# Kernel tuning notes

Measured on AMD Instinct MI355X. Metric: run time of the kernel, lower is better.

## Reference

```python
import jax, jax.numpy as jnp
import numpy as np

B, N, NODE_DIM = 8, 128, 64
L, RES_DIM = 512, 1024
CG, CP = 128, 128
NUM_GNN_STEPS = 3
HID = CG + CP // 2  # interaction hidden = 192


def setup_inputs() -> dict:
    key = jax.random.key(0)
    ks = jax.random.split(key, 20)
    a = (jax.random.uniform(ks[0], (B, N, N)) < 0.05).astype(jnp.float32)
    adj = jnp.clip(a + jnp.swapaxes(a, 1, 2), 0.0, 1.0)
    adj = adj * (1.0 - jnp.eye(N, dtype=jnp.float32))
    nodes = jax.random.normal(ks[1], (B, N, NODE_DIM), dtype=jnp.float32)
    prot = jax.random.normal(ks[2], (B, L, RES_DIM), dtype=jnp.float32)
    s = 0.02
    inp = {
        "adj_mats": adj, "nodes": nodes, "protein_sequences": prot,
        "Wn": jax.random.normal(ks[3], (NODE_DIM, CG)) * s, "bn": jnp.zeros((CG,)),
        "Wg": jax.random.normal(ks[4], (CG, CG)) * s, "bg": jnp.zeros((CG,)),
        "Wr": jax.random.normal(ks[5], (RES_DIM, CP)) * s, "br": jnp.zeros((CP,)),
        "Wa": jax.random.normal(ks[6], (CG + CP, 1)) * s, "ba": jnp.zeros((1,)),
        "W1": jax.random.normal(ks[7], (CG + CP, HID)) * s, "b1": jnp.zeros((HID,)),
        "W2": jax.random.normal(ks[8], (HID, CG)) * s, "b2": jnp.zeros((CG,)),
        "Wo": jax.random.normal(ks[9], (CG, 1)) * s, "bo": jnp.zeros((1,)),
    }
    return inp


def reference(adj_mats, nodes, protein_sequences,
              Wn, bn, Wg, bg, Wr, br, Wa, ba, W1, b1, W2, b2, Wo, bo):
    # node compression: [B,N,CG]
    h = nodes @ Wn + bn
    deg = jnp.clip(jnp.sum(adj_mats, axis=-1), 1.0, None)        # [B,N]
    norm = deg ** -0.5                                           # [B,N]
    for i in range(NUM_GNN_STEPS):
        m = jnp.einsum('bij,bjc->bic', adj_mats, h * norm[..., None])
        h = (m * norm[..., None]) @ Wg + bg
        h = jnp.tanh(h) if i == NUM_GNN_STEPS - 1 else jax.nn.relu(h)
    # residue compression: [B,L,CP]
    r = protein_sequences @ Wr + br
    # MergeSnE1: all-pairs broadcast concat -> [B, N*L, CG+CP]
    cat = jnp.concatenate([
        jnp.broadcast_to(h[:, :, None, :], (B, N, L, CG)),
        jnp.broadcast_to(r[:, None, :, :], (B, N, L, CP)),
    ], axis=-1).reshape(B, N * L, CG + CP)
    # attention: Linear -> Softmax over last dim (size 1 => all ones, faithful)
    attn = jax.nn.softmax(cat @ Wa + ba, axis=-1)                # [B,N*L,1]
    inter = jax.nn.relu(cat @ W1 + b1) @ W2 + b2                 # [B,N*L,CG]
    weighted_sum = jnp.sum(attn * inter, axis=1)                 # [B,CG]
    return weighted_sum @ Wo + bo                                # [B,1]
```

## Files before the change

### kernel.cpp

```cpp
#include <hip/hip_runtime.h>

#define BB 8
#define NN 128
#define ND 64
#define LL 512
#define RD 1024
#define CG 128
#define HID 192

typedef __attribute__((ext_vector_type(8))) short short8;
typedef __attribute__((ext_vector_type(4))) float f32x4;

__device__ __forceinline__ unsigned short f2bf(float x) {
    unsigned u = __builtin_bit_cast(unsigned, x);
    u += 0x7fffu + ((u >> 16) & 1u);
    return (unsigned short)(u >> 16);
}
__device__ __forceinline__ float bf2f(unsigned short h) {
    unsigned u = ((unsigned)h) << 16;
    return __builtin_bit_cast(float, u);
}
#define MFMA __builtin_amdgcn_mfma_f32_16x16x32_bf16

__global__ __launch_bounds__(512, 1) void k_prep(
    const float* __restrict__ adj, const float* __restrict__ nodes,
    const float* __restrict__ Wn, const float* __restrict__ bn,
    const float* __restrict__ Wr, const float* __restrict__ br,
    const float* __restrict__ W1, const float* __restrict__ b1,
    const float* __restrict__ Wg, const float* __restrict__ bg,
    const float* __restrict__ W2, const float* __restrict__ b2,
    const float* __restrict__ Wo, const float* __restrict__ bo,
    unsigned short* __restrict__ WcT, unsigned short* __restrict__ hW1b,
    float* __restrict__ vbuf, float* __restrict__ out)
{
    __shared__ unsigned short hT[NN][136];
    __shared__ unsigned short mbuf[NN][72];
    __shared__ unsigned short WgT[NN][136];
    __shared__ unsigned short W1T[HID][136];
    __shared__ float snorm[NN];
    __shared__ float b1cL[HID];
    __shared__ float sbg[NN];
    int t = threadIdx.x, blk = blockIdx.x;
    int w = t >> 6, l = t & 63, lr = l & 15, ks = l >> 4, lk = ks * 8;
    const float* W1b = W1 + CG * HID;

    if (blk < 16) {
        int r0 = blk * 64;
        #pragma unroll
        for (int q = 0; q < 48; ++q) {
            int e = t + 512 * q;
            int m = e / HID, c = e % HID;
            W1T[c][m] = f2bf(W1[(size_t)(CG + m) * HID + c]);
        }
        int rt = w & 3, jh = w >> 2;
        short8 awr[4];
        #pragma unroll
        for (int kk = 0; kk < 4; ++kk) {
            const float* wp = Wr + (size_t)(r0 + rt * 16 + lr) * CG + kk * 32 + lk;
            float4 q0 = *(const float4*)wp;
            float4 q1 = *(const float4*)(wp + 4);
            unsigned short u[8];
            u[0]=f2bf(q0.x); u[1]=f2bf(q0.y); u[2]=f2bf(q0.z); u[3]=f2bf(q0.w);
            u[4]=f2bf(q1.x); u[5]=f2bf(q1.y); u[6]=f2bf(q1.z); u[7]=f2bf(q1.w);
            awr[kk] = *(const short8*)u;
        }
        __syncthreads();
        #pragma unroll
        for (int jt6 = 0; jt6 < 6; ++jt6) {
            int jt = jh * 6 + jt6;
            f32x4 d = {0.f, 0.f, 0.f, 0.f};
            #pragma unroll
            for (int kk = 0; kk < 4; ++kk) {
                short8 bf = *(const short8*)(&W1T[jt * 16 + lr][kk * 32 + lk]);
                d = MFMA(awr[kk], bf, d, 0, 0, 0);
            }
            unsigned short u[4];
            #pragma unroll
            for (int i = 0; i < 4; ++i) u[i] = f2bf(d[i]);
            *(uint2*)(WcT + (size_t)(jt * 16 + lr) * RD + r0 + rt * 16 + ks * 4) = *(uint2*)u;
        }
        return;
    }
    if (blk == 16) {
        if (t < HID) {
            float s = 0.f;
            #pragma unroll 8
            for (int k = 0; k < CG; ++k) s = fmaf(W2[t * CG + k], Wo[k], s);
            vbuf[t] = s;
        }
        if (t < BB) {
            float s = 0.f;
            for (int k = 0; k < CG; ++k) s = fmaf(b2[k], Wo[k], s);
            out[t] = (float)(NN * LL) * s + bo[0];
        }
        return;
    }

    int b = blk - 17;
    int i0 = w * 16;

    {
        float* dscr = (float*)&mbuf[0][0];
        int row = t >> 2, q4 = t & 3;
        const float* ar = adj + ((size_t)b * NN + row) * NN + q4 * 32;
        float d = 0.f;
        #pragma unroll
        for (int c4 = 0; c4 < 8; ++c4) {
            float4 p = *(const float4*)(ar + c4 * 4);
            d += (p.x + p.y) + (p.z + p.w);
        }
        dscr[row * 4 + q4] = d;
        __syncthreads();
        if (t < NN) {
            snorm[t] = rsqrtf(fmaxf(dscr[t*4] + dscr[t*4+1] + dscr[t*4+2] + dscr[t*4+3], 1.f));
        } else if (t < 320) {
            int j = t - 128;
            float s = b1[j];
            #pragma unroll 8
            for (int m = 0; m < CG; ++m)
                s = fmaf(br[m], W1b[(size_t)m * HID + j], s);
            b1cL[j] = s;
        } else if (t < 448) {
            sbg[t - 320] = bg[t - 320];
        }
        __syncthreads();
    }

    unsigned short* WnT = &mbuf[0][0];
    #pragma unroll
    for (int q = 0; q < 16; ++q) {
        int e = t + 512 * q;
        int c = e & 127, k = e >> 7;
        WnT[c * 72 + k] = f2bf(Wn[(size_t)k * CG + c]);
    }
    #pragma unroll
    for (int q = 0; q < 32; ++q) {
        int e = t + 512 * q;
        int c = e & 127, j = e >> 7;
        WgT[c][j] = f2bf(Wg[(size_t)j * CG + c]);
    }
    #pragma unroll
    for (int q = 0; q < 32; ++q) {
        int e = t + 512 * q;
        int jj = e & 127, k = e >> 7;
        W1T[jj][k] = f2bf(W1[(size_t)k * HID + jj]);
    }
    #pragma unroll
    for (int q = 0; q < 16; ++q) {
        int e = t + 512 * q;
        int jj = 128 + (e & 63), k = e >> 6;
        W1T[jj][k] = f2bf(W1[(size_t)k * HID + jj]);
    }

    short8 af[4];
    {
        float ni = snorm[i0 + lr];
        const float* ar = adj + ((size_t)b * NN + i0 + lr) * NN;
        #pragma unroll
        for (int kk = 0; kk < 4; ++kk) {
            int kb = kk * 32 + lk;
            float4 p0 = *(const float4*)(ar + kb);
            float4 p1 = *(const float4*)(ar + kb + 4);
            unsigned short u[8];
            u[0] = f2bf(p0.x * ni * snorm[kb+0]); u[1] = f2bf(p0.y * ni * snorm[kb+1]);
            u[2] = f2bf(p0.z * ni * snorm[kb+2]); u[3] = f2bf(p0.w * ni * snorm[kb+3]);
            u[4] = f2bf(p1.x * ni * snorm[kb+4]); u[5] = f2bf(p1.y * ni * snorm[kb+5]);
            u[6] = f2bf(p1.z * ni * snorm[kb+6]); u[7] = f2bf(p1.w * ni * snorm[kb+7]);
            af[kk] = *(const short8*)u;
        }
    }
    short8 bnod[2];
    #pragma unroll
    for (int kk = 0; kk < 2; ++kk) {
        const float* np = nodes + ((size_t)b * NN + i0 + lr) * ND + kk * 32 + lk;
        float4 q0 = *(const float4*)np;
        float4 q1 = *(const float4*)(np + 4);
        unsigned short u[8];
        u[0]=f2bf(q0.x); u[1]=f2bf(q0.y); u[2]=f2bf(q0.z); u[3]=f2bf(q0.w);
        u[4]=f2bf(q1.x); u[5]=f2bf(q1.y); u[6]=f2bf(q1.z); u[7]=f2bf(q1.w);
        bnod[kk] = *(const short8*)u;
    }
    __syncthreads();

    #pragma unroll
    for (int ct = 0; ct < 8; ++ct) {
        f32x4 d = {0.f, 0.f, 0.f, 0.f};
        #pragma unroll
        for (int kk = 0; kk < 2; ++kk) {
            short8 afw = *(const short8*)(WnT + (ct * 16 + lr) * 72 + kk * 32 + lk);
            d = MFMA(afw, bnod[kk], d, 0, 0, 0);
        }
        #pragma unroll
        for (int i = 0; i < 4; ++i)
            hT[ct * 16 + ks * 4 + i][i0 + lr] = f2bf(d[i] + bn[ct * 16 + ks * 4 + i]);
    }
    __syncthreads();

    for (int s = 0; s < 3; ++s) {
        f32x4 acc8[8];
        #pragma unroll
        for (int ct = 0; ct < 8; ++ct) acc8[ct] = (f32x4){0.f, 0.f, 0.f, 0.f};
        #pragma unroll
        for (int hf = 0; hf < 2; ++hf) {
            #pragma unroll
            for (int jt = 0; jt < 4; ++jt) {
                int jg = hf * 64 + jt * 16;
                f32x4 d = {0.f, 0.f, 0.f, 0.f};
                #pragma unroll
                for (int kk = 0; kk < 4; ++kk) {
                    short8 bf = *(const short8*)(&hT[jg + lr][kk * 32 + lk]);
                    d = MFMA(af[kk], bf, d, 0, 0, 0);
                }
                #pragma unroll
                for (int i = 0; i < 4; ++i)
                    mbuf[i0 + ks * 4 + i][jt * 16 + lr] = f2bf(d[i]);
            }
            short8 bm[2];
            #pragma unroll
            for (int kk = 0; kk < 2; ++kk)
                bm[kk] = *(const short8*)(&mbuf[i0 + lr][kk * 32 + lk]);
            #pragma unroll
            for (int ct = 0; ct < 8; ++ct) {
                #pragma unroll
                for (int kk = 0; kk < 2; ++kk) {
                    short8 wf = *(const short8*)(&WgT[ct * 16 + lr][hf * 64 + kk * 32 + lk]);
                    if (s < 2)
                        acc8[ct] = MFMA(wf, bm[kk], acc8[ct], 0, 0, 0);
                    else
                        acc8[ct] = MFMA(bm[kk], wf, acc8[ct], 0, 0, 0);
                }
            }
        }
        __syncthreads();
        if (s < 2) {
            #pragma unroll
            for (int ct = 0; ct < 8; ++ct)
                #pragma unroll
                for (int i = 0; i < 4; ++i)
                    hT[ct * 16 + ks * 4 + i][i0 + lr] =
                        f2bf(fmaxf(acc8[ct][i] + sbg[ct * 16 + ks * 4 + i], 0.f));
        } else {
            #pragma unroll
            for (int ct = 0; ct < 8; ++ct)
                #pragma unroll
                for (int i = 0; i < 4; ++i)
                    hT[i0 + ks * 4 + i][ct * 16 + lr] =
                        f2bf(tanhf(acc8[ct][i] + sbg[ct * 16 + lr]));
        }
        __syncthreads();
    }

    {
        short8 bh[4];
        #pragma unroll
        for (int kk = 0; kk < 4; ++kk)
            bh[kk] = *(const short8*)(&hT[i0 + lr][kk * 32 + lk]);
        #pragma unroll
        for (int jjt = 0; jjt < 12; ++jjt) {
            f32x4 d = {0.f, 0.f, 0.f, 0.f};
            #pragma unroll
            for (int kk = 0; kk < 4; ++kk) {
                short8 wf = *(const short8*)(&W1T[jjt * 16 + lr][kk * 32 + lk]);
                d = MFMA(wf, bh[kk], d, 0, 0, 0);
            }
            #pragma unroll
            for (int i = 0; i < 4; ++i) {
                int jj = jjt * 16 + ks * 4 + i;
                hW1b[(size_t)b * HID * NN + jj * NN + i0 + lr] = f2bf(d[i] + b1cL[jj]);
            }
        }
    }
}

__global__ __launch_bounds__(512, 1) void k_gemm(
    const float* __restrict__ prot, const unsigned short* __restrict__ WcT,
    const unsigned short* __restrict__ hW1b, const float* __restrict__ vbuf,
    float* __restrict__ out)
{
    __shared__ unsigned short aT[16 * 1032];
    __shared__ unsigned short h1[HID * 136];
    __shared__ float pbuf[2 * 16 * 192];
    __shared__ float sred[8];
    int t = threadIdx.x, blk = blockIdx.x;
    int b = blk >> 5, lc = blk & 31;
    int w = t >> 6, l = t & 63, lr = l & 15, ks = l >> 4, lk = ks * 8;
    int w2 = w >> 2, wj = w & 3;

    #pragma unroll
    for (int q = 0; q < 4; ++q) {
        int e = t + 512 * q;
        int row = e >> 7;
        int c8 = (e & 127) * 8;
        const float* pr = prot + ((size_t)(b * LL + lc * 16 + row)) * RD + c8;
        float4 p0 = *(const float4*)pr;
        float4 p1 = *(const float4*)(pr + 4);
        unsigned short u[8];
        u[0]=f2bf(p0.x); u[1]=f2bf(p0.y); u[2]=f2bf(p0.z); u[3]=f2bf(p0.w);
        u[4]=f2bf(p1.x); u[5]=f2bf(p1.y); u[6]=f2bf(p1.z); u[7]=f2bf(p1.w);
        *(short8*)(aT + row * 1032 + c8) = *(const short8*)u;
    }
    #pragma unroll
    for (int q = 0; q < 6; ++q) {
        int u8 = t + 512 * q;
        int row = u8 >> 4;
        int n8 = (u8 & 15) * 8;
        short8 v = *(const short8*)(hW1b + (size_t)b * HID * NN + row * NN + n8);
        *(short8*)(h1 + row * 136 + n8) = v;
    }
    float v0 = vbuf[wj * 48 + lr];
    float v1 = vbuf[wj * 48 + 16 + lr];
    float v2 = vbuf[wj * 48 + 32 + lr];
    __syncthreads();

    f32x4 a0 = {0.f,0.f,0.f,0.f}, a1 = a0, a2 = a0;
    {
        const unsigned short* ap = aT + lr * 1032 + w2 * 512 + lk;
        const unsigned short* bp = WcT + (size_t)(wj * 48 + lr) * RD + w2 * 512 + lk;
        #pragma unroll 4
        for (int k0 = 0; k0 < 512; k0 += 32) {
            short8 av = *(const short8*)(ap + k0);
            short8 b0 = *(const short8*)(bp + k0);
            short8 b1 = *(const short8*)(bp + 16 * RD + k0);
            short8 b2 = *(const short8*)(bp + 32 * RD + k0);
            a0 = MFMA(av, b0, a0, 0, 0, 0);
            a1 = MFMA(av, b1, a1, 0, 0, 0);
            a2 = MFMA(av, b2, a2, 0, 0, 0);
        }
    }
    #pragma unroll
    for (int i = 0; i < 4; ++i) {
        int r = ks * 4 + i;
        pbuf[(w2 * 16 + r) * 192 + wj * 48 + lr]      = a0[i];
        pbuf[(w2 * 16 + r) * 192 + wj * 48 + 16 + lr] = a1[i];
        pbuf[(w2 * 16 + r) * 192 + wj * 48 + 32 + lr] = a2[i];
    }
    __syncthreads();
    float rw0[4], rw1[4], rw2[4];
    #pragma unroll
    for (int i = 0; i < 4; ++i) {
        int r = ks * 4 + i;
        rw0[i] = pbuf[r * 192 + wj*48 + lr]      + pbuf[(16 + r) * 192 + wj*48 + lr];
        rw1[i] = pbuf[r * 192 + wj*48 + 16 + lr] + pbuf[(16 + r) * 192 + wj*48 + 16 + lr];
        rw2[i] = pbuf[r * 192 + wj*48 + 32 + lr] + pbuf[(16 + r) * 192 + wj*48 + 32 + lr];
    }

    const unsigned short* h0p = h1 + (wj * 48 + lr) * 136 + w2 * 64;
    const unsigned short* h1p = h0p + 16 * 136;
    const unsigned short* h2p = h0p + 32 * 136;
    float s = 0.f;
    #pragma unroll 2
    for (int n0 = 0; n0 < 64; n0 += 4) {
        unsigned short e0[4], e1[4], e2[4];
        *(uint2*)e0 = *(const uint2*)(h0p + n0);
        *(uint2*)e1 = *(const uint2*)(h1p + n0);
        *(uint2*)e2 = *(const uint2*)(h2p + n0);
        #pragma unroll
        for (int q = 0; q < 4; ++q) {
            float hh0 = bf2f(e0[q]), hh1 = bf2f(e1[q]), hh2 = bf2f(e2[q]);
            #pragma unroll
            for (int i = 0; i < 4; ++i) {
                s = fmaf(v0, fmaxf(rw0[i] + hh0, 0.f), s);
                s = fmaf(v1, fmaxf(rw1[i] + hh1, 0.f), s);
                s = fmaf(v2, fmaxf(rw2[i] + hh2, 0.f), s);
            }
        }
    }
    for (int off = 32; off; off >>= 1) s += __shfl_down(s, off);
    if (l == 0) sred[w] = s;
    __syncthreads();
    if (t == 0) {
        float tot = ((sred[0] + sred[1]) + (sred[2] + sred[3]))
                  + ((sred[4] + sred[5]) + (sred[6] + sred[7]));
        atomicAdd(&out[b], tot);
    }
}

extern "C" void kernel_launch(void* const* d_in, const int* in_sizes, int n_in,
                              void* d_out, int out_size, void* d_ws, size_t ws_size,
                              hipStream_t stream)
{
    const float* adj   = (const float*)d_in[0];
    const float* nodes = (const float*)d_in[1];
    const float* prot  = (const float*)d_in[2];
    const float* Wn    = (const float*)d_in[3];
    const float* bn    = (const float*)d_in[4];
    const float* Wg    = (const float*)d_in[5];
    const float* bg    = (const float*)d_in[6];
    const float* Wr    = (const float*)d_in[7];
    const float* br    = (const float*)d_in[8];
    const float* W1    = (const float*)d_in[11];
    const float* b1    = (const float*)d_in[12];
    const float* W2    = (const float*)d_in[13];
    const float* b2    = (const float*)d_in[14];
    const float* Wo    = (const float*)d_in[15];
    const float* bo    = (const float*)d_in[16];

    float* ws     = (float*)d_ws;
    float* vbuf   = ws;
    unsigned short* hW1b = (unsigned short*)(ws + 192);
    unsigned short* WcT  = hW1b + (size_t)BB * HID * NN;
    float* out    = (float*)d_out;

    hipLaunchKernelGGL(k_prep, dim3(25), dim3(512), 0, stream,
                       adj, nodes, Wn, bn, Wr, br, W1, b1, Wg, bg,
                       W2, b2, Wo, bo, WcT, hW1b, vbuf, out);
    hipLaunchKernelGGL(k_gemm, dim3(256), dim3(512), 0, stream,
                       prot, WcT, hW1b, vbuf, out);
}
```

Measured before the change: 55.18 us.

## Merge prep and GEMM kernels into one cooperative kernel with grid sync

```diff
diff --git a/kernel.cpp b/kernel.cpp
--- a/kernel.cpp
+++ b/kernel.cpp
@@ -1,4 +1,7 @@
 #include <hip/hip_runtime.h>
+#include <hip/hip_cooperative_groups.h>
+
+namespace cg = cooperative_groups;
 
 #define BB 8
 #define NN 128
@@ -22,8 +25,18 @@
 }
 #define MFMA __builtin_amdgcn_mfma_f32_16x16x32_bf16
 
-__global__ __launch_bounds__(512, 1) void k_prep(
+#define OFF_PBUF  33024
+#define OFF_H1    57600
+#define OFF_MBUF  34816
+#define OFF_WGT   53248
+#define OFF_W1T   88064
+#define OFF_SNORM 140288
+#define OFF_B1C   140800
+#define OFF_SBG   141568
+
+__global__ __launch_bounds__(512, 1) void kmega(
     const float* __restrict__ adj, const float* __restrict__ nodes,
+    const float* __restrict__ prot,
     const float* __restrict__ Wn, const float* __restrict__ bn,
     const float* __restrict__ Wr, const float* __restrict__ br,
     const float* __restrict__ W1, const float* __restrict__ b1,
@@ -33,24 +46,42 @@
     unsigned short* __restrict__ WcT, unsigned short* __restrict__ hW1b,
     float* __restrict__ vbuf, float* __restrict__ out)
 {
-    __shared__ unsigned short hT[NN][136];
-    __shared__ unsigned short mbuf[NN][72];
-    __shared__ unsigned short WgT[NN][136];
-    __shared__ unsigned short W1T[HID][136];
-    __shared__ float snorm[NN];
-    __shared__ float b1cL[HID];
-    __shared__ float sbg[NN];
+    __shared__ char smem[142080];
+    __shared__ float sred[8];
     int t = threadIdx.x, blk = blockIdx.x;
     int w = t >> 6, l = t & 63, lr = l & 15, ks = l >> 4, lk = ks * 8;
     const float* W1b = W1 + CG * HID;
 
+    unsigned short* aT = (unsigned short*)smem;
+    float* pbuf = (float*)(smem + OFF_PBUF);
+    unsigned short* h1 = (unsigned short*)(smem + OFF_H1);
+
+    int bg_ = blk >> 5, lc = blk & 31;
+
+    if (blk < 17 || blk >= 25) {
+        #pragma unroll
+        for (int q = 0; q < 4; ++q) {
+            int e = t + 512 * q;
+            int row = e >> 7;
+            int c8 = (e & 127) * 8;
+            const float* pr = prot + ((size_t)(bg_ * LL + lc * 16 + row)) * RD + c8;
+            float4 p0 = *(const float4*)pr;
+            float4 p1 = *(const float4*)(pr + 4);
+            unsigned short u[8];
+            u[0]=f2bf(p0.x); u[1]=f2bf(p0.y); u[2]=f2bf(p0.z); u[3]=f2bf(p0.w);
+            u[4]=f2bf(p1.x); u[5]=f2bf(p1.y); u[6]=f2bf(p1.z); u[7]=f2bf(p1.w);
+            *(short8*)(aT + row * 1032 + c8) = *(const short8*)u;
+        }
+    }
+
     if (blk < 16) {
+        unsigned short (*W1Tw)[136] = (unsigned short(*)[136])(smem + OFF_H1);
         int r0 = blk * 64;
         #pragma unroll
         for (int q = 0; q < 48; ++q) {
             int e = t + 512 * q;
             int m = e / HID, c = e % HID;
-            W1T[c][m] = f2bf(W1[(size_t)(CG + m) * HID + c]);
+            W1Tw[c][m] = f2bf(W1[(size_t)(CG + m) * HID + c]);
         }
         int rt = w & 3, jh = w >> 2;
         short8 awr[4];
@@ -71,7 +102,7 @@
             f32x4 d = {0.f, 0.f, 0.f, 0.f};
             #pragma unroll
             for (int kk = 0; kk < 4; ++kk) {
-                short8 bf = *(const short8*)(&W1T[jt * 16 + lr][kk * 32 + lk]);
+                short8 bf = *(const short8*)(&W1Tw[jt * 16 + lr][kk * 32 + lk]);
                 d = MFMA(awr[kk], bf, d, 0, 0, 0);
             }
             unsigned short u[4];
@@ -79,9 +110,7 @@
             for (int i = 0; i < 4; ++i) u[i] = f2bf(d[i]);
             *(uint2*)(WcT + (size_t)(jt * 16 + lr) * RD + r0 + rt * 16 + ks * 4) = *(uint2*)u;
         }
-        return;
-    }
-    if (blk == 16) {
+    } else if (blk == 16) {
         if (t < HID) {
             float s = 0.f;
             #pragma unroll 8
@@ -93,220 +122,216 @@
             for (int k = 0; k < CG; ++k) s = fmaf(b2[k], Wo[k], s);
             out[t] = (float)(NN * LL) * s + bo[0];
         }
-        return;
-    }
-
-    int b = blk - 17;
-    int i0 = w * 16;
-
-    {
-        float* dscr = (float*)&mbuf[0][0];
-        int row = t >> 2, q4 = t & 3;
-        const float* ar = adj + ((size_t)b * NN + row) * NN + q4 * 32;
-        float d = 0.f;
-        #pragma unroll
-        for (int c4 = 0; c4 < 8; ++c4) {
-            float4 p = *(const float4*)(ar + c4 * 4);
-            d += (p.x + p.y) + (p.z + p.w);
-        }
-        dscr[row * 4 + q4] = d;
+    } else if (blk < 25) {
+        unsigned short (*hT)[136] = (unsigned short(*)[136])smem;
+        unsigned short (*mbuf)[72] = (unsigned short(*)[72])(smem + OFF_MBUF);
+        unsigned short (*WgT)[136] = (unsigned short(*)[136])(smem + OFF_WGT);
+        unsigned short (*W1T)[136] = (unsigned short(*)[136])(smem + OFF_W1T);
+        float* snorm = (float*)(smem + OFF_SNORM);
+        float* b1cL  = (float*)(smem + OFF_B1C);
+        float* sbg   = (float*)(smem + OFF_SBG);
+        int b = blk - 17;
+        int i0 = w * 16;
+
+        {
+            float* dscr = (float*)&mbuf[0][0];
+            int row = t >> 2, q4 = t & 3;
+            const float* ar = adj + ((size_t)b * NN + row) * NN + q4 * 32;
+            float d = 0.f;
+            #pragma unroll
+            for (int c4 = 0; c4 < 8; ++c4) {
+                float4 p = *(const float4*)(ar + c4 * 4);
+                d += (p.x + p.y) + (p.z + p.w);
+            }
+            dscr[row * 4 + q4] = d;
+            __syncthreads();
+            if (t < NN) {
+                snorm[t] = rsqrtf(fmaxf(dscr[t*4] + dscr[t*4+1] + dscr[t*4+2] + dscr[t*4+3], 1.f));
+            } else if (t < 320) {
+                int j = t - 128;
+                float s = b1[j];
+                #pragma unroll 8
+                for (int m = 0; m < CG; ++m)
+                    s = fmaf(br[m], W1b[(size_t)m * HID + j], s);
+                b1cL[j] = s;
+            } else if (t < 448) {
+                sbg[t - 320] = bg[t - 320];
+            }
+            __syncthreads();
+        }
+
+        unsigned short* WnT = &mbuf[0][0];
+        #pragma unroll
+        for (int q = 0; q < 16; ++q) {
+            int e = t + 512 * q;
+            int c = e & 127, k = e >> 7;
+            WnT[c * 72 + k] = f2bf(Wn[(size_t)k * CG + c]);
+        }
+        #pragma unroll
+        for (int q = 0; q < 32; ++q) {
+            int e = t + 512 * q;
+            int c = e & 127, j = e >> 7;
+            WgT[c][j] = f2bf(Wg[(size_t)j * CG + c]);
+        }
+        #pragma unroll
+        for (int q = 0; q < 32; ++q) {
+            int e = t + 512 * q;
+            int jj = e & 127, k = e >> 7;
+            W1T[jj][k] = f2bf(W1[(size_t)k * HID + jj]);
+        }
+        #pragma unroll
+        for (int q = 0; q < 16; ++q) {
+            int e = t + 512 * q;
+            int jj = 128 + (e & 63), k = e >> 6;
+            W1T[jj][k] = f2bf(W1[(size_t)k * HID + jj]);
+        }
+
+        short8 af[4];
+        {
+            float ni = snorm[i0 + lr];
+            const float* ar = adj + ((size_t)b * NN + i0 + lr) * NN;
+            #pragma unroll
+            for (int kk = 0; kk < 4; ++kk) {
+                int kb = kk * 32 + lk;
+                float4 p0 = *(const float4*)(ar + kb);
+                float4 p1 = *(const float4*)(ar + kb + 4);
+                unsigned short u[8];
+                u[0] = f2bf(p0.x * ni * snorm[kb+0]); u[1] = f2bf(p0.y * ni * snorm[kb+1]);
+                u[2] = f2bf(p0.z * ni * snorm[kb+2]); u[3] = f2bf(p0.w * ni * snorm[kb+3]);
+                u[4] = f2bf(p1.x * ni * snorm[kb+4]); u[5] = f2bf(p1.y * ni * snorm[kb+5]);
+                u[6] = f2bf(p1.z * ni * snorm[kb+6]); u[7] = f2bf(p1.w * ni * snorm[kb+7]);
+                af[kk] = *(const short8*)u;
+            }
+        }
+        short8 bnod[2];
+        #pragma unroll
+        for (int kk = 0; kk < 2; ++kk) {
+            const float* np = nodes + ((size_t)b * NN + i0 + lr) * ND + kk * 32 + lk;
+            float4 q0 = *(const float4*)np;
+            float4 q1 = *(const float4*)(np + 4);
+            unsigned short u[8];
+            u[0]=f2bf(q0.x); u[1]=f2bf(q0.y); u[2]=f2bf(q0.z); u[3]=f2bf(q0.w);
+            u[4]=f2bf(q1.x); u[5]=f2bf(q1.y); u[6]=f2bf(q1.z); u[7]=f2bf(q1.w);
+            bnod[kk] = *(const short8*)u;
+        }
         __syncthreads();
-        if (t < NN) {
-            snorm[t] = rsqrtf(fmaxf(dscr[t*4] + dscr[t*4+1] + dscr[t*4+2] + dscr[t*4+3], 1.f));
-        } else if (t < 320) {
-            int j = t - 128;
-            float s = b1[j];
-            #pragma unroll 8
-            for (int m = 0; m < CG; ++m)
-                s = fmaf(br[m], W1b[(size_t)m * HID + j], s);
-            b1cL[j] = s;
-        } else if (t < 448) {
-            sbg[t - 320] = bg[t - 320];
+
+        #pragma unroll
+        for (int ct = 0; ct < 8; ++ct) {
+            f32x4 d = {0.f, 0.f, 0.f, 0.f};
+            #pragma unroll
+            for (int kk = 0; kk < 2; ++kk) {
+                short8 afw = *(const short8*)(WnT + (ct * 16 + lr) * 72 + kk * 32 + lk);
+                d = MFMA(afw, bnod[kk], d, 0, 0, 0);
+            }
+            #pragma unroll
+            for (int i = 0; i < 4; ++i)
+                hT[ct * 16 + ks * 4 + i][i0 + lr] = f2bf(d[i] + bn[ct * 16 + ks * 4 + i]);
         }
         __syncthreads();
-    }
-
-    unsigned short* WnT = &mbuf[0][0];
-    #pragma unroll
-    for (int q = 0; q < 16; ++q) {
-        int e = t + 512 * q;
-        int c = e & 127, k = e >> 7;
-        WnT[c * 72 + k] = f2bf(Wn[(size_t)k * CG + c]);
-    }
-    #pragma unroll
-    for (int q = 0; q < 32; ++q) {
-        int e = t + 512 * q;
-        int c = e & 127, j = e >> 7;
-        WgT[c][j] = f2bf(Wg[(size_t)j * CG + c]);
-    }
-    #pragma unroll
-    for (int q = 0; q < 32; ++q) {
-        int e = t + 512 * q;
-        int jj = e & 127, k = e >> 7;
-        W1T[jj][k] = f2bf(W1[(size_t)k * HID + jj]);
-    }
-    #pragma unroll
-    for (int q = 0; q < 16; ++q) {
-        int e = t + 512 * q;
-        int jj = 128 + (e & 63), k = e >> 6;
-        W1T[jj][k] = f2bf(W1[(size_t)k * HID + jj]);
-    }
-
-    short8 af[4];
-    {
-        float ni = snorm[i0 + lr];
-        const float* ar = adj + ((size_t)b * NN + i0 + lr) * NN;
-        #pragma unroll
-        for (int kk = 0; kk < 4; ++kk) {
-            int kb = kk * 32 + lk;
-            float4 p0 = *(const float4*)(ar + kb);
-            float4 p1 = *(const float4*)(ar + kb + 4);
+
+        for (int s = 0; s < 3; ++s) {
+            f32x4 acc8[8];
+            #pragma unroll
+            for (int ct = 0; ct < 8; ++ct) acc8[ct] = (f32x4){0.f, 0.f, 0.f, 0.f};
+            #pragma unroll
+            for (int hf = 0; hf < 2; ++hf) {
+                #pragma unroll
+                for (int jt = 0; jt < 4; ++jt) {
+                    int jg = hf * 64 + jt * 16;
+                    f32x4 d = {0.f, 0.f, 0.f, 0.f};
+                    #pragma unroll
+                    for (int kk = 0; kk < 4; ++kk) {
+                        short8 bf = *(const short8*)(&hT[jg + lr][kk * 32 + lk]);
+                        d = MFMA(af[kk], bf, d, 0, 0, 0);
+                    }
+                    #pragma unroll
+                    for (int i = 0; i < 4; ++i)
+                        mbuf[i0 + ks * 4 + i][jt * 16 + lr] = f2bf(d[i]);
+                }
+                short8 bm[2];
+                #pragma unroll
+                for (int kk = 0; kk < 2; ++kk)
+                    bm[kk] = *(const short8*)(&mbuf[i0 + lr][kk * 32 + lk]);
+                #pragma unroll
+                for (int ct = 0; ct < 8; ++ct) {
+                    #pragma unroll
+                    for (int kk = 0; kk < 2; ++kk) {
+                        short8 wf = *(const short8*)(&WgT[ct * 16 + lr][hf * 64 + kk * 32 + lk]);
+                        if (s < 2)
+                            acc8[ct] = MFMA(wf, bm[kk], acc8[ct], 0, 0, 0);
+                        else
+                            acc8[ct] = MFMA(bm[kk], wf, acc8[ct], 0, 0, 0);
+                    }
+                }
+            }
+            __syncthreads();
+            if (s < 2) {
+                #pragma unroll
+                for (int ct = 0; ct < 8; ++ct)
+                    #pragma unroll
+                    for (int i = 0; i < 4; ++i)
+                        hT[ct * 16 + ks * 4 + i][i0 + lr] =
+                            f2bf(fmaxf(acc8[ct][i] + sbg[ct * 16 + ks * 4 + i], 0.f));
+            } else {
+                #pragma unroll
+                for (int ct = 0; ct < 8; ++ct)
+                    #pragma unroll
+                    for (int i = 0; i < 4; ++i)
+                        hT[i0 + ks * 4 + i][ct * 16 + lr] =
+                            f2bf(tanhf(acc8[ct][i] + sbg[ct * 16 + lr]));
+            }
+            __syncthreads();
+        }
+
+        {
+            short8 bh[4];
+            #pragma unroll
+            for (int kk = 0; kk < 4; ++kk)
+                bh[kk] = *(const short8*)(&hT[i0 + lr][kk * 32 + lk]);
+            #pragma unroll
+            for (int jjt = 0; jjt < 12; ++jjt) {
+                f32x4 d = {0.f, 0.f, 0.f, 0.f};
+                #pragma unroll
+                for (int kk = 0; kk < 4; ++kk) {
+                    short8 wf = *(const short8*)(&W1T[jjt * 16 + lr][kk * 32 + lk]);
+                    d = MFMA(wf, bh[kk], d, 0, 0, 0);
+                }
+                #pragma unroll
+                for (int i = 0; i < 4; ++i) {
+                    int jj = jjt * 16 + ks * 4 + i;
+                    hW1b[(size_t)b * HID * NN + jj * NN + i0 + lr] = f2bf(d[i] + b1cL[jj]);
+                }
+            }
+        }
+    }
+
+    cg::this_grid().sync();
+
+    if (blk >= 17 && blk < 25) {
+        #pragma unroll
+        for (int q = 0; q < 4; ++q) {
+            int e = t + 512 * q;
+            int row = e >> 7;
+            int c8 = (e & 127) * 8;
+            const float* pr = prot + ((size_t)(bg_ * LL + lc * 16 + row)) * RD + c8;
+            float4 p0 = *(const float4*)pr;
+            float4 p1 = *(const float4*)(pr + 4);
             unsigned short u[8];
-            u[0] = f2bf(p0.x * ni * snorm[kb+0]); u[1] = f2bf(p0.y * ni * snorm[kb+1]);
-            u[2] = f2bf(p0.z * ni * snorm[kb+2]); u[3] = f2bf(p0.w * ni * snorm[kb+3]);
-            u[4] = f2bf(p1.x * ni * snorm[kb+4]); u[5] = f2bf(p1.y * ni * snorm[kb+5]);
-            u[6] = f2bf(p1.z * ni * snorm[kb+6]); u[7] = f2bf(p1.w * ni * snorm[kb+7]);
-            af[kk] = *(const short8*)u;
-        }
-    }
-    short8 bnod[2];
-    #pragma unroll
-    for (int kk = 0; kk < 2; ++kk) {
-        const float* np = nodes + ((size_t)b * NN + i0 + lr) * ND + kk * 32 + lk;
-        float4 q0 = *(const float4*)np;
-        float4 q1 = *(const float4*)(np + 4);
-        unsigned short u[8];
-        u[0]=f2bf(q0.x); u[1]=f2bf(q0.y); u[2]=f2bf(q0.z); u[3]=f2bf(q0.w);
-        u[4]=f2bf(q1.x); u[5]=f2bf(q1.y); u[6]=f2bf(q1.z); u[7]=f2bf(q1.w);
-        bnod[kk] = *(const short8*)u;
-    }
-    __syncthreads();
-
-    #pragma unroll
-    for (int ct = 0; ct < 8; ++ct) {
-        f32x4 d = {0.f, 0.f, 0.f, 0.f};
-        #pragma unroll
-        for (int kk = 0; kk < 2; ++kk) {
-            short8 afw = *(const short8*)(WnT + (ct * 16 + lr) * 72 + kk * 32 + lk);
-            d = MFMA(afw, bnod[kk], d, 0, 0, 0);
-        }
-        #pragma unroll
-        for (int i = 0; i < 4; ++i)
-            hT[ct * 16 + ks * 4 + i][i0 + lr] = f2bf(d[i] + bn[ct * 16 + ks * 4 + i]);
-    }
-    __syncthreads();
-
-    for (int s = 0; s < 3; ++s) {
-        f32x4 acc8[8];
-        #pragma unroll
-        for (int ct = 0; ct < 8; ++ct) acc8[ct] = (f32x4){0.f, 0.f, 0.f, 0.f};
-        #pragma unroll
-        for (int hf = 0; hf < 2; ++hf) {
-            #pragma unroll
-            for (int jt = 0; jt < 4; ++jt) {
-                int jg = hf * 64 + jt * 16;
-                f32x4 d = {0.f, 0.f, 0.f, 0.f};
-                #pragma unroll
-                for (int kk = 0; kk < 4; ++kk) {
-                    short8 bf = *(const short8*)(&hT[jg + lr][kk * 32 + lk]);
-                    d = MFMA(af[kk], bf, d, 0, 0, 0);
-                }
-                #pragma unroll
-                for (int i = 0; i < 4; ++i)
-                    mbuf[i0 + ks * 4 + i][jt * 16 + lr] = f2bf(d[i]);
-            }
-            short8 bm[2];
-            #pragma unroll
-            for (int kk = 0; kk < 2; ++kk)
-                bm[kk] = *(const short8*)(&mbuf[i0 + lr][kk * 32 + lk]);
-            #pragma unroll
-            for (int ct = 0; ct < 8; ++ct) {
-                #pragma unroll
-                for (int kk = 0; kk < 2; ++kk) {
-                    short8 wf = *(const short8*)(&WgT[ct * 16 + lr][hf * 64 + kk * 32 + lk]);
-                    if (s < 2)
-                        acc8[ct] = MFMA(wf, bm[kk], acc8[ct], 0, 0, 0);
-                    else
-                        acc8[ct] = MFMA(bm[kk], wf, acc8[ct], 0, 0, 0);
-                }
-            }
-        }
-        __syncthreads();
-        if (s < 2) {
-            #pragma unroll
-            for (int ct = 0; ct < 8; ++ct)
-                #pragma unroll
-                for (int i = 0; i < 4; ++i)
-                    hT[ct * 16 + ks * 4 + i][i0 + lr] =
-                        f2bf(fmaxf(acc8[ct][i] + sbg[ct * 16 + ks * 4 + i], 0.f));
-        } else {
-            #pragma unroll
-            for (int ct = 0; ct < 8; ++ct)
-                #pragma unroll
-                for (int i = 0; i < 4; ++i)
-                    hT[i0 + ks * 4 + i][ct * 16 + lr] =
-                        f2bf(tanhf(acc8[ct][i] + sbg[ct * 16 + lr]));
-        }
-        __syncthreads();
-    }
-
-    {
-        short8 bh[4];
-        #pragma unroll
-        for (int kk = 0; kk < 4; ++kk)
-            bh[kk] = *(const short8*)(&hT[i0 + lr][kk * 32 + lk]);
-        #pragma unroll
-        for (int jjt = 0; jjt < 12; ++jjt) {
-            f32x4 d = {0.f, 0.f, 0.f, 0.f};
-            #pragma unroll
-            for (int kk = 0; kk < 4; ++kk) {
-                short8 wf = *(const short8*)(&W1T[jjt * 16 + lr][kk * 32 + lk]);
-                d = MFMA(wf, bh[kk], d, 0, 0, 0);
-            }
-            #pragma unroll
-            for (int i = 0; i < 4; ++i) {
-                int jj = jjt * 16 + ks * 4 + i;
-                hW1b[(size_t)b * HID * NN + jj * NN + i0 + lr] = f2bf(d[i] + b1cL[jj]);
-            }
-        }
-    }
-}
-
-__global__ __launch_bounds__(512, 1) void k_gemm(
-    const float* __restrict__ prot, const unsigned short* __restrict__ WcT,
-    const unsigned short* __restrict__ hW1b, const float* __restrict__ vbuf,
-    float* __restrict__ out)
-{
-    __shared__ unsigned short aT[16 * 1032];
-    __shared__ unsigned short h1[HID * 136];
-    __shared__ float pbuf[2 * 16 * 192];
-    __shared__ float sred[8];
-    int t = threadIdx.x, blk = blockIdx.x;
-    int b = blk >> 5, lc = blk & 31;
-    int w = t >> 6, l = t & 63, lr = l & 15, ks = l >> 4, lk = ks * 8;
-    int w2 = w >> 2, wj = w & 3;
-
-    #pragma unroll
-    for (int q = 0; q < 4; ++q) {
-        int e = t + 512 * q;
-        int row = e >> 7;
-        int c8 = (e & 127) * 8;
-        const float* pr = prot + ((size_t)(b * LL + lc * 16 + row)) * RD + c8;
-        float4 p0 = *(const float4*)pr;
-        float4 p1 = *(const float4*)(pr + 4);
-        unsigned short u[8];
-        u[0]=f2bf(p0.x); u[1]=f2bf(p0.y); u[2]=f2bf(p0.z); u[3]=f2bf(p0.w);
-        u[4]=f2bf(p1.x); u[5]=f2bf(p1.y); u[6]=f2bf(p1.z); u[7]=f2bf(p1.w);
-        *(short8*)(aT + row * 1032 + c8) = *(const short8*)u;
+            u[0]=f2bf(p0.x); u[1]=f2bf(p0.y); u[2]=f2bf(p0.z); u[3]=f2bf(p0.w);
+            u[4]=f2bf(p1.x); u[5]=f2bf(p1.y); u[6]=f2bf(p1.z); u[7]=f2bf(p1.w);
+            *(short8*)(aT + row * 1032 + c8) = *(const short8*)u;
+        }
     }
     #pragma unroll
     for (int q = 0; q < 6; ++q) {
         int u8 = t + 512 * q;
         int row = u8 >> 4;
         int n8 = (u8 & 15) * 8;
-        short8 v = *(const short8*)(hW1b + (size_t)b * HID * NN + row * NN + n8);
+        short8 v = *(const short8*)(hW1b + (size_t)bg_ * HID * NN + row * NN + n8);
         *(short8*)(h1 + row * 136 + n8) = v;
     }
+    int w2 = w >> 2, wj = w & 3;
     float v0 = vbuf[wj * 48 + lr];
     float v1 = vbuf[wj * 48 + 16 + lr];
     float v2 = vbuf[wj * 48 + 32 + lr];
@@ -320,11 +345,11 @@
         for (int k0 = 0; k0 < 512; k0 += 32) {
             short8 av = *(const short8*)(ap + k0);
             short8 b0 = *(const short8*)(bp + k0);
-            short8 b1 = *(const short8*)(bp + 16 * RD + k0);
-            short8 b2 = *(const short8*)(bp + 32 * RD + k0);
+            short8 b1v = *(const short8*)(bp + 16 * RD + k0);
+            short8 b2v = *(const short8*)(bp + 32 * RD + k0);
             a0 = MFMA(av, b0, a0, 0, 0, 0);
-            a1 = MFMA(av, b1, a1, 0, 0, 0);
-            a2 = MFMA(av, b2, a2, 0, 0, 0);
+            a1 = MFMA(av, b1v, a1, 0, 0, 0);
+            a2 = MFMA(av, b2v, a2, 0, 0, 0);
         }
     }
     #pragma unroll
@@ -371,7 +396,7 @@
     if (t == 0) {
         float tot = ((sred[0] + sred[1]) + (sred[2] + sred[3]))
                   + ((sred[4] + sred[5]) + (sred[6] + sred[7]));
-        atomicAdd(&out[b], tot);
+        atomicAdd(&out[bg_], tot);
     }
 }
 
@@ -399,11 +424,15 @@
     float* vbuf   = ws;
     unsigned short* hW1b = (unsigned short*)(ws + 192);
     unsigned short* WcT  = hW1b + (size_t)BB * HID * NN;
-    float* out    = (float*)d_out;
-
-    hipLaunchKernelGGL(k_prep, dim3(25), dim3(512), 0, stream,
-                       adj, nodes, Wn, bn, Wr, br, W1, b1, Wg, bg,
-                       W2, b2, Wo, bo, WcT, hW1b, vbuf, out);
-    hipLaunchKernelGGL(k_gemm, dim3(256), dim3(512), 0, stream,
-                       prot, WcT, hW1b, vbuf, out);
+    float* outp   = (float*)d_out;
+
+    void* kargs[] = {
+        (void*)&adj, (void*)&nodes, (void*)&prot,
+        (void*)&Wn, (void*)&bn, (void*)&Wr, (void*)&br,
+        (void*)&W1, (void*)&b1, (void*)&Wg, (void*)&bg,
+        (void*)&W2, (void*)&b2, (void*)&Wo, (void*)&bo,
+        (void*)&WcT, (void*)&hW1b, (void*)&vbuf, (void*)&outp
+    };
+    hipLaunchCooperativeKernel((const void*)kmega, dim3(256), dim3(512),
+                               kargs, 0, stream);
 }
```

Result: slower. 86.61 us (+57.0%).
